# Performance work log

Hardware: AMD Instinct MI355X
Metric: run time of the kernel (lower is better)

## Reference

```python
import jax, jax.numpy as jnp
import numpy as np

INPUT_DIM, HIDDEN_DIM, OUTPUT_DIM = 256, 64, 64
N_NODES, N_EDGES = 100000, 1200000


def setup_inputs() -> dict:
    key = jax.random.key(0)
    k1, k2, k3, k4 = jax.random.split(key, 4)
    x = jax.random.normal(k1, (N_NODES, INPUT_DIM), dtype=jnp.float32)
    edge_index = jax.random.randint(k2, (2, N_EDGES), 0, N_NODES, dtype=jnp.int64)
    # torch Linear weight layout: [out_features, in_features], xavier_uniform init
    def xavier(k, shape):
        fan_out, fan_in = shape
        lim = float(np.sqrt(6.0 / (fan_in + fan_out)))
        return jax.random.uniform(k, shape, minval=-lim, maxval=lim, dtype=jnp.float32)
    W1 = xavier(k3, (HIDDEN_DIM, INPUT_DIM))
    b1 = jnp.zeros((HIDDEN_DIM,), dtype=jnp.float32)
    W2 = xavier(k4, (OUTPUT_DIM, HIDDEN_DIM))
    b2 = jnp.zeros((OUTPUT_DIM,), dtype=jnp.float32)
    return {"x": x, "edge_index": edge_index, "W1": W1, "b1": b1, "W2": W2, "b2": b2}


def reference(x, edge_index, W1, b1, W2, b2):
    N = x.shape[0]
    loops = jnp.arange(N, dtype=edge_index.dtype)
    # GCNConv default: add self-loops, symmetric deg^-1/2 normalization
    src = jnp.concatenate([edge_index[0], loops])  # message sources (x_j)
    dst = jnp.concatenate([edge_index[1], loops])  # aggregation targets
    deg = jax.ops.segment_sum(jnp.ones_like(src, dtype=x.dtype), dst, num_segments=N)
    dinv = jnp.where(deg > 0, jax.lax.rsqrt(jnp.maximum(deg, 1e-12)), 0.0)
    norm = dinv[src] * dinv[dst]  # [E+N]

    def gcn_layer(h, W, b):
        h = h @ W.T                      # dense linear transform [N, out]
        msg = h[src] * norm[:, None]     # gather + scale [E+N, out]
        agg = jax.ops.segment_sum(msg, dst, num_segments=N)  # scatter-add
        return agg + b

    h = jax.nn.relu(gcn_layer(x, W1, b1))
    out = jax.nn.relu(gcn_layer(h, W2, b2))
    return out
```

## Files before the change

### kernel.cpp

```cpp
#include <hip/hip_runtime.h>

static constexpr int NN  = 100000;
static constexpr int NE  = 1200000;
static constexpr int KIN = 256;
static constexpr int HID = 64;

static constexpr int BSH   = 7;
static constexpr int NPB   = 1 << BSH;
static constexpr int NB    = (NN + NPB - 1) / NPB;
static constexpr int CAP   = 4096;
static constexpr int CHUNK = 8192;
static constexpr int NBK   = (NE + CHUNK - 1) / CHUNK;

typedef __attribute__((ext_vector_type(8))) __bf16 bf16v8;
typedef __attribute__((ext_vector_type(4))) float f32x4;

__device__ __forceinline__ float bf2f(unsigned short u) {
  return __uint_as_float(((unsigned int)u) << 16);
}
__device__ __forceinline__ unsigned short f2bf(float f) {
  unsigned int b = __float_as_uint(f);
  return (unsigned short)((b + 0x7FFFu + ((b >> 16) & 1u)) >> 16);
}

__global__ void k_wconv2z(const float* __restrict__ W1, __bf16* __restrict__ Whi1, __bf16* __restrict__ Wlo1,
                          const float* __restrict__ W2, __bf16* __restrict__ Whi2, __bf16* __restrict__ Wlo2,
                          int* __restrict__ gcur) {
  int i = blockIdx.x * 256 + threadIdx.x;
  constexpr int n1 = HID * KIN;
  if (i < n1) {
    float v = W1[i];
    __bf16 h = (__bf16)v;
    Whi1[i] = h;
    Wlo1[i] = (__bf16)(v - (float)h);
  } else if (i < n1 + HID * HID) {
    int j = i - n1;
    float v = W2[j];
    __bf16 h = (__bf16)v;
    Whi2[j] = h;
    Wlo2[j] = (__bf16)(v - (float)h);
  }
  if (i < NB) gcur[i] = 0;
}

__global__ void __launch_bounds__(256) k_bin1p(const int* __restrict__ ed, int* __restrict__ gcur,
                                               unsigned* __restrict__ binned) {
  __shared__ int lcnt[NB];
  __shared__ int lbase[NB];
  int t = threadIdx.x, blk = blockIdx.x;
  for (int i = t; i < NB; i += 256) lcnt[i] = 0;
  __syncthreads();
  int base = blk * CHUNK;
  #pragma unroll
  for (int it = 0; it < CHUNK / 256; ++it) {
    int e = base + it * 256 + t;
    if (e < NE) atomicAdd(&lcnt[ed[NE + e] >> BSH], 1);
  }
  __syncthreads();
  for (int i = t; i < NB; i += 256) {
    int c = lcnt[i];
    lbase[i] = (c > 0) ? atomicAdd(&gcur[i], c) : 0;
    lcnt[i] = 0;
  }
  __syncthreads();
  #pragma unroll
  for (int it = 0; it < CHUNK / 256; ++it) {
    int e = base + it * 256 + t;
    if (e < NE) {
      int src = ed[e];
      int dst = ed[NE + e];
      int b = dst >> BSH;
      int r = atomicAdd(&lcnt[b], 1);
      binned[(size_t)b * CAP + lbase[b] + r] = (unsigned)src | ((unsigned)(dst & (NPB - 1)) << 17);
    }
  }
}

__global__ void __launch_bounds__(256) k_degcsr(const unsigned* __restrict__ binned,
                                                const int* __restrict__ gcur,
                                                int* __restrict__ deg, float* __restrict__ dinv,
                                                int* __restrict__ rp, int* __restrict__ csr) {
  __shared__ int d[NPB];
  __shared__ int sc[NPB];
  __shared__ int cur[NPB];
  int t = threadIdx.x, b = blockIdx.x;
  if (t < NPB) { d[t] = 0; cur[t] = 0; }
  __syncthreads();
  const int n = gcur[b];
  const unsigned* win = binned + (size_t)b * CAP;
  for (int i = t; i < n; i += 256) atomicAdd(&d[win[i] >> 17], 1);
  __syncthreads();
  if (t < NPB) sc[t] = d[t];
  __syncthreads();
  #pragma unroll
  for (int off = 1; off < NPB; off <<= 1) {
    int x = (t < NPB && t >= off) ? sc[t - off] : 0;
    __syncthreads();
    if (t < NPB) sc[t] += x;
    __syncthreads();
  }
  if (t < NPB) {
    int node = b * NPB + t;
    if (node < NN) {
      deg[node] = d[t];
      dinv[node] = rsqrtf((float)(d[t] + 1));
      rp[node] = b * CAP + sc[t] - d[t];
    }
  }
  __syncthreads();
  for (int i = t; i < n; i += 256) {
    unsigned u = win[i];
    int src = (int)(u & 0x1FFFFu);
    int dl  = (int)(u >> 17);
    int r = atomicAdd(&cur[dl], 1);
    csr[(size_t)b * CAP + (sc[dl] - d[dl]) + r] = src;
  }
}

template<int K, int MODE>
__global__ void __launch_bounds__(256, 4)
k_gemm(const float* __restrict__ X, const __bf16* __restrict__ Whi, const __bf16* __restrict__ Wlo,
       const float* __restrict__ dinv, const float* __restrict__ bias, void* __restrict__ Yv) {
  constexpr int KT = 32;
  constexpr int NT = K / KT;
  constexpr int LS = 40;
  constexpr int CS = 68;
  __shared__ __align__(16) char smem[4 * 64 * LS * 2];
  __bf16* xh = (__bf16*)smem;
  __bf16* xl = xh + 64 * LS;
  __bf16* wh = xl + 64 * LS;
  __bf16* wl = wh + 64 * LS;
  float*  cl = (float*)smem;

  const int t = threadIdx.x;
  const int l = t & 63;
  const int wc = (t >> 6) * 16;
  const int rowbase = blockIdx.x * 64;

  f32x4 acc[4];
  #pragma unroll
  for (int rt = 0; rt < 4; ++rt) acc[rt] = (f32x4){0.f, 0.f, 0.f, 0.f};

  const int sr = t >> 2;
  const int kc = (t & 3) * 8;

  for (int kt = 0; kt < NT; ++kt) {
    __syncthreads();
    {
      int gr = rowbase + sr;
      float4 v0 = make_float4(0.f, 0.f, 0.f, 0.f), v1 = v0;
      if (gr < NN) {
        const float* xp = X + (size_t)gr * K + kt * KT + kc;
        v0 = *reinterpret_cast<const float4*>(xp);
        v1 = *reinterpret_cast<const float4*>(xp + 4);
      }
      float e[8] = {v0.x, v0.y, v0.z, v0.w, v1.x, v1.y, v1.z, v1.w};
      bf16v8 hv, lv;
      #pragma unroll
      for (int j = 0; j < 8; ++j) {
        __bf16 h = (__bf16)e[j];
        hv[j] = h;
        lv[j] = (__bf16)(e[j] - (float)h);
      }
      *reinterpret_cast<bf16v8*>(&xh[sr * LS + kc]) = hv;
      *reinterpret_cast<bf16v8*>(&xl[sr * LS + kc]) = lv;
      *reinterpret_cast<bf16v8*>(&wh[sr * LS + kc]) =
          *reinterpret_cast<const bf16v8*>(Whi + (size_t)sr * K + kt * KT + kc);
      *reinterpret_cast<bf16v8*>(&wl[sr * LS + kc]) =
          *reinterpret_cast<const bf16v8*>(Wlo + (size_t)sr * K + kt * KT + kc);
    }
    __syncthreads();

    const int bo = (wc + (l & 15)) * LS + (l >> 4) * 8;
    bf16v8 bh = *reinterpret_cast<const bf16v8*>(&wh[bo]);
    bf16v8 bl = *reinterpret_cast<const bf16v8*>(&wl[bo]);
    #pragma unroll
    for (int rt = 0; rt < 4; ++rt) {
      const int ao = (rt * 16 + (l & 15)) * LS + (l >> 4) * 8;
      bf16v8 ah = *reinterpret_cast<const bf16v8*>(&xh[ao]);
      bf16v8 al = *reinterpret_cast<const bf16v8*>(&xl[ao]);
      acc[rt] = __builtin_amdgcn_mfma_f32_16x16x32_bf16(ah, bh, acc[rt], 0, 0, 0);
      acc[rt] = __builtin_amdgcn_mfma_f32_16x16x32_bf16(al, bh, acc[rt], 0, 0, 0);
      acc[rt] = __builtin_amdgcn_mfma_f32_16x16x32_bf16(ah, bl, acc[rt], 0, 0, 0);
    }
  }

  __syncthreads();
  #pragma unroll
  for (int rt = 0; rt < 4; ++rt)
    #pragma unroll
    for (int j = 0; j < 4; ++j)
      cl[(rt * 16 + (l >> 4) * 4 + j) * CS + wc + (l & 15)] = acc[rt][j];
  __syncthreads();

  const int r = t >> 2, cc = (t & 3) * 16;
  const int grow = rowbase + r;
  if (grow < NN) {
    if (MODE == 0) {
      float dv = dinv[grow];
      bf16v8 o0, o1;
      #pragma unroll
      for (int j = 0; j < 8; ++j) o0[j] = (__bf16)(cl[r * CS + cc + j] * dv);
      #pragma unroll
      for (int j = 0; j < 8; ++j) o1[j] = (__bf16)(cl[r * CS + cc + 8 + j] * dv);
      __bf16* yp = (__bf16*)Yv + (size_t)grow * HID + cc;
      *reinterpret_cast<bf16v8*>(yp) = o0;
      *reinterpret_cast<bf16v8*>(yp + 8) = o1;
    } else {
      float* yp = (float*)Yv + (size_t)grow * HID + cc;
      #pragma unroll
      for (int c4 = 0; c4 < 4; ++c4) {
        float4 o;
        o.x = fmaxf(cl[r * CS + cc + c4 * 4 + 0] + bias[cc + c4 * 4 + 0], 0.f);
        o.y = fmaxf(cl[r * CS + cc + c4 * 4 + 1] + bias[cc + c4 * 4 + 1], 0.f);
        o.z = fmaxf(cl[r * CS + cc + c4 * 4 + 2] + bias[cc + c4 * 4 + 2], 0.f);
        o.w = fmaxf(cl[r * CS + cc + c4 * 4 + 3] + bias[cc + c4 * 4 + 3], 0.f);
        *reinterpret_cast<float4*>(yp + c4 * 4) = o;
      }
    }
  }
}

template<int MODE>
__global__ void __launch_bounds__(256, 8)
k_agg(const unsigned short* __restrict__ T, const int* __restrict__ csr,
      const int* __restrict__ rp, const int* __restrict__ deg,
      const float* __restrict__ dinv, const float* __restrict__ bias,
      void* __restrict__ Ov) {
  int node = blockIdx.x * 4 + (threadIdx.x >> 6);
  int lane = threadIdx.x & 63;
  float acc = bf2f(T[(size_t)node * HID + lane]);
  int start = rp[node];
  int len = deg[node];
  for (int base = 0; base < len; base += 64) {
    int m = min(64, len - base);
    int idx = (lane < m) ? csr[start + base + lane] : 0;
    for (int c0 = 0; c0 < m; c0 += 16) {
      float part = 0.f;
      #pragma unroll
      for (int i = 0; i < 16; ++i) {
        int e = c0 + i;
        int s = __shfl(idx, e & 63);
        float v = bf2f(T[(size_t)s * HID + lane]);
        part += (e < m) ? v : 0.f;
      }
      acc += part;
    }
  }
  float dv = dinv[node];
  if (MODE == 0) {
    float h = dv * fmaxf(fmaf(dv, acc, bias[lane]), 0.f);
    ((unsigned short*)Ov)[(size_t)node * HID + lane] = f2bf(h);
  } else {
    ((float*)Ov)[(size_t)node * HID + lane] = dv * acc;
  }
}

extern "C" void kernel_launch(void* const* d_in, const int* in_sizes, int n_in,
                              void* d_out, int out_size, void* d_ws, size_t ws_size,
                              hipStream_t stream) {
  const float* x  = (const float*)d_in[0];
  const int*   ed = (const int*)d_in[1];
  const float* W1 = (const float*)d_in[2];
  const float* b1 = (const float*)d_in[3];
  const float* W2 = (const float*)d_in[4];
  const float* b2 = (const float*)d_in[5];
  float* out = (float*)d_out;

  char* ws = (char*)d_ws;
  size_t off = 0;
  auto alloc = [&](size_t bytes) {
    char* p = ws + off;
    off = (off + bytes + 255) & ~(size_t)255;
    return p;
  };
  int*      deg    = (int*)alloc((size_t)NN * 4);
  float*    dinv   = (float*)alloc((size_t)NN * 4);
  int*      rp     = (int*)alloc((size_t)NN * 4);
  int*      gcur   = (int*)alloc((size_t)NB * 4);
  unsigned* binned = (unsigned*)alloc((size_t)NB * CAP * 4);
  int*      csr    = (int*)alloc((size_t)NB * CAP * 4);
  float*    A      = (float*)alloc((size_t)NN * HID * 4);
  __bf16*   Whi1   = (__bf16*)alloc((size_t)HID * KIN * 2);
  __bf16*   Wlo1   = (__bf16*)alloc((size_t)HID * KIN * 2);
  __bf16*   Whi2   = (__bf16*)alloc((size_t)HID * HID * 2);
  __bf16*   Wlo2   = (__bf16*)alloc((size_t)HID * HID * 2);
  unsigned short* Hp = (unsigned short*)d_out;

  k_wconv2z<<<(HID * KIN + HID * HID + 255) / 256, 256, 0, stream>>>(W1, Whi1, Wlo1, W2, Whi2, Wlo2, gcur);
  k_bin1p<<<NBK, 256, 0, stream>>>(ed, gcur, binned);
  k_degcsr<<<NB, 256, 0, stream>>>(binned, gcur, deg, dinv, rp, csr);

  const int GB = (NN + 63) / 64;

  k_gemm<KIN, 0><<<GB, 256, 0, stream>>>(x, Whi1, Wlo1, dinv, b1, A);
  k_agg<0><<<NN / 4, 256, 0, stream>>>((const unsigned short*)A, csr, rp, deg, dinv, b1, Hp);

  k_agg<1><<<NN / 4, 256, 0, stream>>>(Hp, csr, rp, deg, dinv, b2, A);
  k_gemm<HID, 1><<<GB, 256, 0, stream>>>((const float*)A, Whi2, Wlo2, dinv, b2, out);
}
```

Measured before the change: 157.3 us.

## Fuse second-layer aggregation with the 64x64 MFMA GEMM and epilogue

```diff
diff --git a/kernel.cpp b/kernel.cpp
--- a/kernel.cpp
+++ b/kernel.cpp
@@ -221,12 +221,11 @@
   }
 }
 
-template<int MODE>
 __global__ void __launch_bounds__(256, 8)
 k_agg(const unsigned short* __restrict__ T, const int* __restrict__ csr,
       const int* __restrict__ rp, const int* __restrict__ deg,
       const float* __restrict__ dinv, const float* __restrict__ bias,
-      void* __restrict__ Ov) {
+      unsigned short* __restrict__ Ov) {
   int node = blockIdx.x * 4 + (threadIdx.x >> 6);
   int lane = threadIdx.x & 63;
   float acc = bf2f(T[(size_t)node * HID + lane]);
@@ -248,11 +247,99 @@
     }
   }
   float dv = dinv[node];
-  if (MODE == 0) {
-    float h = dv * fmaxf(fmaf(dv, acc, bias[lane]), 0.f);
-    ((unsigned short*)Ov)[(size_t)node * HID + lane] = f2bf(h);
-  } else {
-    ((float*)Ov)[(size_t)node * HID + lane] = dv * acc;
+  float h = dv * fmaxf(fmaf(dv, acc, bias[lane]), 0.f);
+  Ov[(size_t)node * HID + lane] = f2bf(h);
+}
+
+__global__ void __launch_bounds__(256, 8)
+k_aggemm(const unsigned short* __restrict__ T, const int* __restrict__ csr,
+         const int* __restrict__ rp, const int* __restrict__ deg,
+         const float* __restrict__ dinv,
+         const __bf16* __restrict__ Whi2, const __bf16* __restrict__ Wlo2,
+         const float* __restrict__ bias, float* __restrict__ out) {
+  constexpr int LS = 72;
+  constexpr int CS = 68;
+  __shared__ __align__(16) char smem[2 * 64 * LS * 2];
+  __bf16* gh = (__bf16*)smem;
+  __bf16* gl = gh + 64 * LS;
+  float*  cl = (float*)smem;
+
+  const int t = threadIdx.x;
+  const int l = t & 63;
+  const int w = t >> 6;
+  const int rowbase = blockIdx.x * 64;
+
+  for (int i = 0; i < 16; ++i) {
+    int node = rowbase + w * 16 + i;
+    float gv = 0.f;
+    if (node < NN) {
+      float acc = bf2f(T[(size_t)node * HID + l]);
+      int start = rp[node];
+      int len = deg[node];
+      for (int base = 0; base < len; base += 64) {
+        int m = min(64, len - base);
+        int idx = (l < m) ? csr[start + base + l] : 0;
+        for (int c0 = 0; c0 < m; c0 += 16) {
+          float part = 0.f;
+          #pragma unroll
+          for (int j = 0; j < 16; ++j) {
+            int e = c0 + j;
+            int s = __shfl(idx, e & 63);
+            float v = bf2f(T[(size_t)s * HID + l]);
+            part += (e < m) ? v : 0.f;
+          }
+          acc += part;
+        }
+      }
+      gv = dinv[node] * acc;
+    }
+    __bf16 h = (__bf16)gv;
+    int r = w * 16 + i;
+    gh[r * LS + l] = h;
+    gl[r * LS + l] = (__bf16)(gv - (float)h);
+  }
+  __syncthreads();
+
+  const int wc = w * 16;
+  f32x4 acc[4];
+  #pragma unroll
+  for (int rt = 0; rt < 4; ++rt) acc[rt] = (f32x4){0.f, 0.f, 0.f, 0.f};
+  #pragma unroll
+  for (int kc = 0; kc < 2; ++kc) {
+    const size_t wo = (size_t)(wc + (l & 15)) * HID + kc * 32 + (l >> 4) * 8;
+    bf16v8 bh = *reinterpret_cast<const bf16v8*>(Whi2 + wo);
+    bf16v8 bl = *reinterpret_cast<const bf16v8*>(Wlo2 + wo);
+    #pragma unroll
+    for (int rt = 0; rt < 4; ++rt) {
+      const int ao = (rt * 16 + (l & 15)) * LS + kc * 32 + (l >> 4) * 8;
+      bf16v8 ah = *reinterpret_cast<const bf16v8*>(&gh[ao]);
+      bf16v8 al = *reinterpret_cast<const bf16v8*>(&gl[ao]);
+      acc[rt] = __builtin_amdgcn_mfma_f32_16x16x32_bf16(ah, bh, acc[rt], 0, 0, 0);
+      acc[rt] = __builtin_amdgcn_mfma_f32_16x16x32_bf16(al, bh, acc[rt], 0, 0, 0);
+      acc[rt] = __builtin_amdgcn_mfma_f32_16x16x32_bf16(ah, bl, acc[rt], 0, 0, 0);
+    }
+  }
+  __syncthreads();
+  #pragma unroll
+  for (int rt = 0; rt < 4; ++rt)
+    #pragma unroll
+    for (int j = 0; j < 4; ++j)
+      cl[(rt * 16 + (l >> 4) * 4 + j) * CS + wc + (l & 15)] = acc[rt][j];
+  __syncthreads();
+
+  const int r = t >> 2, cc = (t & 3) * 16;
+  const int grow = rowbase + r;
+  if (grow < NN) {
+    float* yp = out + (size_t)grow * HID + cc;
+    #pragma unroll
+    for (int c4 = 0; c4 < 4; ++c4) {
+      float4 o;
+      o.x = fmaxf(cl[r * CS + cc + c4 * 4 + 0] + bias[cc + c4 * 4 + 0], 0.f);
+      o.y = fmaxf(cl[r * CS + cc + c4 * 4 + 1] + bias[cc + c4 * 4 + 1], 0.f);
+      o.z = fmaxf(cl[r * CS + cc + c4 * 4 + 2] + bias[cc + c4 * 4 + 2], 0.f);
+      o.w = fmaxf(cl[r * CS + cc + c4 * 4 + 3] + bias[cc + c4 * 4 + 3], 0.f);
+      *reinterpret_cast<float4*>(yp + c4 * 4) = o;
+    }
   }
 }
 
@@ -280,12 +367,12 @@
   int*      gcur   = (int*)alloc((size_t)NB * 4);
   unsigned* binned = (unsigned*)alloc((size_t)NB * CAP * 4);
   int*      csr    = (int*)alloc((size_t)NB * CAP * 4);
-  float*    A      = (float*)alloc((size_t)NN * HID * 4);
+  unsigned short* T1 = (unsigned short*)alloc((size_t)NN * HID * 2);
+  unsigned short* Hp = (unsigned short*)alloc((size_t)NN * HID * 2);
   __bf16*   Whi1   = (__bf16*)alloc((size_t)HID * KIN * 2);
   __bf16*   Wlo1   = (__bf16*)alloc((size_t)HID * KIN * 2);
   __bf16*   Whi2   = (__bf16*)alloc((size_t)HID * HID * 2);
   __bf16*   Wlo2   = (__bf16*)alloc((size_t)HID * HID * 2);
-  unsigned short* Hp = (unsigned short*)d_out;
 
   k_wconv2z<<<(HID * KIN + HID * HID + 255) / 256, 256, 0, stream>>>(W1, Whi1, Wlo1, W2, Whi2, Wlo2, gcur);
   k_bin1p<<<NBK, 256, 0, stream>>>(ed, gcur, binned);
@@ -293,9 +380,8 @@
 
   const int GB = (NN + 63) / 64;
 
-  k_gemm<KIN, 0><<<GB, 256, 0, stream>>>(x, Whi1, Wlo1, dinv, b1, A);
-  k_agg<0><<<NN / 4, 256, 0, stream>>>((const unsigned short*)A, csr, rp, deg, dinv, b1, Hp);
-
-  k_agg<1><<<NN / 4, 256, 0, stream>>>(Hp, csr, rp, deg, dinv, b2, A);
-  k_gemm<HID, 1><<<GB, 256, 0, stream>>>((const float*)A, Whi2, Wlo2, dinv, b2, out);
-}
+  k_gemm<KIN, 0><<<GB, 256, 0, stream>>>(x, Whi1, Wlo1, dinv, b1, (void*)T1);
+  k_agg<<<NN / 4, 256, 0, stream>>>(T1, csr, rp, deg, dinv, b1, Hp);
+
+  k_aggemm<<<GB, 256, 0, stream>>>(Hp, csr, rp, deg, dinv, Whi2, Wlo2, b2, out);
+}
```

After: 154.3 us. About the same (-1.9%).
